# Kernel tuning notes

Hardware: AMD Instinct MI355X
Metric: run time of the kernel (lower is better)

## Reference

```python
import jax, jax.numpy as jnp
import numpy as np

# ---- constants mirroring init_kwargs ----
S = 128          # sheet_units
KA = 25          # aff_cf_units
C = 2            # aff_cf_channels
KL = 25          # lat_cf_units
EXC = 9          # exc_units
DA = 1           # aff_cf_dilation
DL = 1           # lat_cf_dilation
HOMEO_TARGET = 0.04
STRENGTH = 1.0

# ---- radial helper masks (get_circle / get_radial_cos) ----
def _dist(n):
    g = jnp.arange(n, dtype=jnp.float32) - (n - 1) / 2.0
    return jnp.sqrt(g[:, None] ** 2 + g[None, :] ** 2)

def _circle(n, r):
    return (_dist(n) < r).astype(jnp.float32)

def _rcos(n, wl):
    return jnp.cos(_dist(n) * jnp.pi / wl)

# afferent envelope: [C*KA*KA], channel-major like torch repeat+view
_ae = _rcos(KA, KA) ** 2 * _circle(KA, KA / 2)
_ae = _ae / _ae.max()
AFF_ENV = jnp.tile(_ae.reshape(1, KA * KA), (C, 1)).reshape(C * KA * KA)

# lateral (LRI) envelope: [KL*KL]
_inh = _rcos(KL, EXC / DL) ** 2 * _circle(KL, EXC / (2 * DL))
_le = _rcos(KL, KL) ** 2 * (1.0 - _inh) * _circle(KL, KL / 2)
LRI_ENV = (_le / _le.max()).reshape(KL * KL)

def _unfold(x, k, dil):
    """x: [C,H,W] -> patches [L, C*k*k], torch F.unfold ordering (C slowest)."""
    Cc, H, W = x.shape
    out = H - dil * (k - 1)
    idx = jnp.arange(out)[:, None] + dil * jnp.arange(k)[None, :]  # [out,k]
    p = x[:, idx, :]          # [C,out,k,W]
    p = p[:, :, :, idx]       # [C,out,k,out,k]
    p = p.transpose(1, 3, 0, 2, 4)  # [out_i,out_j,C,ki,kj]
    return p.reshape(out * out, Cc * k * k)

def setup_inputs() -> dict:
    key = jax.random.key(0)
    k1, k2 = jax.random.split(key)
    in_size = S + DA * (KA - 1)  # 152
    x = jax.random.uniform(k1, (1, C, in_size, in_size), dtype=jnp.float32)
    rfs = jax.random.uniform(k2, (S * S, C * KA * KA, 1), dtype=jnp.float32)
    rfs = rfs / rfs.sum(1, keepdims=True)
    lat_weights = jnp.ones((S * S, KL * KL, 1), jnp.float32) / (KL * KL)
    adathresh = jnp.zeros((1, 1, S, S), jnp.float32)
    return {"x": x, "rfs": rfs, "lat_weights": lat_weights, "adathresh": adathresh}

def _forward(x, rfs, lat_weights, adathresh):
    relu = jax.nn.relu
    rfs = relu(rfs)                 # no_grad positive clamp of params
    lw = relu(lat_weights)
    # afferent: unfold + envelope + per-pixel dot (bmm with [L,F,1])
    tiles = _unfold(x[0], KA, DA) * AFF_ENV[None, :]          # [L, C*KA*KA]
    raw_aff = jnp.einsum('lf,lf->l', tiles, rfs[:, :, 0]).reshape(S, S)
    aff = jax.lax.stop_gradient(raw_aff) - adathresh[0, 0]
    lat = relu(aff)
    # lateral inhibition: pad so unfold yields S*S positions
    p = DL * (KL - 1) // 2
    lt = _unfold(jnp.pad(lat, p)[None], KL, DL) * LRI_ENV[None, :]  # [L, KL*KL]
    lat_neg = jnp.einsum('lf,lf->l', lt, jax.lax.stop_gradient(lw)[:, :, 0]).reshape(S, S)
    lat = lat - lat_neg
    lat = jnp.tanh(relu(lat * STRENGTH + aff))
    # hebbian lateral correlations term (learning_flag path)
    lt2 = _unfold(jnp.pad(lat, p, constant_values=HOMEO_TARGET)[None], KL, DL) * LRI_ENV[None, :]
    weighted = lt2 * lat.reshape(S * S, 1)
    lat_correlations = jnp.einsum('lf,lf->', weighted, lw[:, :, 0])
    return (raw_aff.reshape(1, 1, S, S), lat.reshape(1, 1, S, S),
            lat_correlations, tiles[:, None, :])

def reference(x, rfs, lat_weights, adathresh):
    return _forward(x, rfs, lat_weights, adathresh)
```

## Files before the change

### kernel.cpp

```cpp
#include <hip/hip_runtime.h>
#include <math.h>

#define S 128
#define KA 25
#define KL 25
#define PATCH 625
#define FEAT 1250
#define PI_F 3.14159265358979323846f

#define WS_ENV 0
#define WS_LAT0 640
#define WS_PART 17024

__global__ __launch_bounds__(256) void k_tiles_aff(const float* __restrict__ x,
                                                   const float* __restrict__ rfs,
                                                   const float* __restrict__ ada,
                                                   float* __restrict__ raw_aff,
                                                   float* __restrict__ tiles,
                                                   float* __restrict__ ws) {
    __shared__ float s_ae[PATCH];
    __shared__ float s_part[8];
    const int tid = threadIdx.x;
    const int lane = tid & 63;
    const int wv = tid >> 6;

    for (int i = tid; i < PATCH; i += 256) {
        float di = (float)(i / KA) - 12.0f;
        float dj = (float)(i % KA) - 12.0f;
        float d = sqrtf(di * di + dj * dj);
        float v = 0.0f;
        if (d < 12.5f) { float c = cosf(d * (PI_F / 25.0f)); v = c * c; }
        s_ae[i] = v;
    }
    __syncthreads();

    const int p = blockIdx.x;
    const long pbase = (long)p * 2500;
    const float4* __restrict__ rfs4 = (const float4*)(rfs + pbase);
    float4* __restrict__ st4 = (float4*)(tiles + pbase - 1);

    float acc0 = 0.0f, acc1 = 0.0f;
    for (int k = tid; k < 625; k += 256) {
        float t[5];
#pragma unroll
        for (int e = 0; e < 5; ++e) {
            int fp = 4 * k - 1 + e;
            int u = fp + 1250;
            int li_ = u / 1250;
            int f = u - 1250 * li_;
            int l = 2 * p + li_ - 1;
            if (l < 0) l = 0;
            int c = f >= 625;
            int r = f - 625 * c;
            int ki = r / 25;
            int kj = r - 25 * ki;
            int li = l >> 7, lj = l & 127;
            t[e] = x[c * (152 * 152) + (li + ki) * 152 + (lj + kj)] * s_ae[r];
        }
        st4[k] = make_float4(t[0], t[1], t[2], t[3]);
        float4 rv = rfs4[k];
        if (4 * k + 3 < 1250) {
            acc0 += t[1] * fmaxf(rv.x, 0.f) + t[2] * fmaxf(rv.y, 0.f)
                  + t[3] * fmaxf(rv.z, 0.f) + t[4] * fmaxf(rv.w, 0.f);
        } else if (4 * k >= 1250) {
            acc1 += t[1] * fmaxf(rv.x, 0.f) + t[2] * fmaxf(rv.y, 0.f)
                  + t[3] * fmaxf(rv.z, 0.f) + t[4] * fmaxf(rv.w, 0.f);
        } else {
            acc0 += t[1] * fmaxf(rv.x, 0.f) + t[2] * fmaxf(rv.y, 0.f);
            acc1 += t[3] * fmaxf(rv.z, 0.f) + t[4] * fmaxf(rv.w, 0.f);
        }
    }

    if (p == 8191 && tid == 0) {
        tiles[pbase + 2499] = x[152 * 152 + 151 * 152 + 151] * s_ae[624];
    }

    for (int off = 32; off > 0; off >>= 1) {
        acc0 += __shfl_down(acc0, off);
        acc1 += __shfl_down(acc1, off);
    }
    if (lane == 0) { s_part[wv] = acc0; s_part[4 + wv] = acc1; }
    __syncthreads();
    if (tid == 0) {
        float ra0 = s_part[0] + s_part[1] + s_part[2] + s_part[3];
        float ra1 = s_part[4] + s_part[5] + s_part[6] + s_part[7];
        int l0 = 2 * p;
        raw_aff[l0] = ra0;
        raw_aff[l0 + 1] = ra1;
        ws[WS_LAT0 + l0] = fmaxf(ra0 - ada[l0], 0.0f);
        ws[WS_LAT0 + l0 + 1] = fmaxf(ra1 - ada[l0 + 1], 0.0f);
    }

    if (blockIdx.x == 0) {
        __syncthreads();
        float m = 0.0f;
        for (int i = tid; i < PATCH; i += 256) {
            float di = (float)(i / KL) - 12.0f;
            float dj = (float)(i % KL) - 12.0f;
            float d = sqrtf(di * di + dj * dj);
            float v = 0.0f;
            if (d < 12.5f) {
                float c1 = cosf(d * (PI_F / 25.0f));
                float inh = 0.0f;
                if (d < 4.5f) { float c2 = cosf(d * (PI_F / 9.0f)); inh = c2 * c2; }
                v = c1 * c1 * (1.0f - inh);
            }
            s_ae[i] = v;
            m = fmaxf(m, v);
        }
        for (int off = 32; off > 0; off >>= 1) m = fmaxf(m, __shfl_down(m, off));
        if (lane == 0) s_part[wv] = m;
        __syncthreads();
        float inv = 1.0f / fmaxf(fmaxf(s_part[0], s_part[1]),
                                 fmaxf(s_part[2], s_part[3]));
        for (int i = tid; i < PATCH; i += 256) ws[WS_ENV + i] = s_ae[i] * inv;
    }
}

__global__ __launch_bounds__(256) void k_lat(const float* __restrict__ raw_aff,
                                             const float* __restrict__ ada,
                                             const float* __restrict__ lw,
                                             float* __restrict__ latf,
                                             const float* __restrict__ ws) {
    __shared__ float s_le[PATCH];
    const int tid = threadIdx.x;
    for (int i = tid; i < PATCH; i += 256) s_le[i] = ws[WS_ENV + i];
    __syncthreads();

    const int lane = tid & 63;
    const int wv = tid >> 6;
    const int q = blockIdx.x * 4 + wv;
    const int l0 = q * 4;
    const float4* __restrict__ lw4 = (const float4*)(lw + (long)q * 2500);
    const float* __restrict__ lat0 = ws + WS_LAT0;

    float a0 = 0.f, a1 = 0.f, a2 = 0.f, a3 = 0.f;
    for (int k = lane; k < 625; k += 64) {
        float4 w4 = lw4[k];
        float w[4] = { w4.x, w4.y, w4.z, w4.w };
#pragma unroll
        for (int e = 0; e < 4; ++e) {
            int fp = 4 * k + e;
            int li_ = fp / 625;
            int r = fp - 625 * li_;
            int ki = r / 25;
            int kj = r - 25 * ki;
            int l = l0 + li_;
            int ri = (l >> 7) + ki - 12;
            int rj = (l & 127) + kj - 12;
            float lv = 0.0f;
            if (ri >= 0 && ri < S && rj >= 0 && rj < S) lv = lat0[ri * S + rj];
            float contrib = lv * s_le[r] * fmaxf(w[e], 0.0f);
            a0 += (li_ == 0) ? contrib : 0.0f;
            a1 += (li_ == 1) ? contrib : 0.0f;
            a2 += (li_ == 2) ? contrib : 0.0f;
            a3 += (li_ == 3) ? contrib : 0.0f;
        }
    }
    for (int off = 32; off > 0; off >>= 1) {
        a0 += __shfl_down(a0, off); a1 += __shfl_down(a1, off);
        a2 += __shfl_down(a2, off); a3 += __shfl_down(a3, off);
    }
    if (lane == 0) {
        float acc[4] = { a0, a1, a2, a3 };
#pragma unroll
        for (int j = 0; j < 4; ++j) {
            int l = l0 + j;
            float aff_l = raw_aff[l] - ada[l];
            float v = fmaxf(aff_l, 0.0f) - acc[j] + aff_l;
            latf[l] = tanhf(fmaxf(v, 0.0f));
        }
    }
}

__global__ __launch_bounds__(256) void k_corr(const float* __restrict__ latf,
                                              const float* __restrict__ lw,
                                              float* __restrict__ ws) {
    __shared__ float s_le[PATCH];
    __shared__ float s_part[4];
    const int tid = threadIdx.x;
    for (int i = tid; i < PATCH; i += 256) s_le[i] = ws[WS_ENV + i];
    __syncthreads();

    const int lane = tid & 63;
    const int wv = tid >> 6;
    const int q = blockIdx.x * 4 + wv;
    const int l0 = q * 4;
    const float4* __restrict__ lw4 = (const float4*)(lw + (long)q * 2500);

    float a0 = 0.f, a1 = 0.f, a2 = 0.f, a3 = 0.f;
    for (int k = lane; k < 625; k += 64) {
        float4 w4 = lw4[k];
        float w[4] = { w4.x, w4.y, w4.z, w4.w };
#pragma unroll
        for (int e = 0; e < 4; ++e) {
            int fp = 4 * k + e;
            int li_ = fp / 625;
            int r = fp - 625 * li_;
            int ki = r / 25;
            int kj = r - 25 * ki;
            int l = l0 + li_;
            int ri = (l >> 7) + ki - 12;
            int rj = (l & 127) + kj - 12;
            float lv = 0.04f;
            if (ri >= 0 && ri < S && rj >= 0 && rj < S) lv = latf[ri * S + rj];
            float contrib = lv * s_le[r] * fmaxf(w[e], 0.0f);
            a0 += (li_ == 0) ? contrib : 0.0f;
            a1 += (li_ == 1) ? contrib : 0.0f;
            a2 += (li_ == 2) ? contrib : 0.0f;
            a3 += (li_ == 3) ? contrib : 0.0f;
        }
    }
    for (int off = 32; off > 0; off >>= 1) {
        a0 += __shfl_down(a0, off); a1 += __shfl_down(a1, off);
        a2 += __shfl_down(a2, off); a3 += __shfl_down(a3, off);
    }
    if (lane == 0) {
        s_part[wv] = a0 * latf[l0] + a1 * latf[l0 + 1]
                   + a2 * latf[l0 + 2] + a3 * latf[l0 + 3];
    }
    __syncthreads();
    if (tid == 0)
        ws[WS_PART + blockIdx.x] = s_part[0] + s_part[1] + s_part[2] + s_part[3];
}

__global__ __launch_bounds__(256) void k_reduce(const float* __restrict__ ws,
                                                float* __restrict__ corr) {
    __shared__ float s_part[4];
    const int tid = threadIdx.x;
    const int lane = tid & 63;
    const int wv = tid >> 6;
    float acc = 0.0f;
    for (int i = tid; i < 1024; i += 256) acc += ws[WS_PART + i];
    for (int off = 32; off > 0; off >>= 1) acc += __shfl_down(acc, off);
    if (lane == 0) s_part[wv] = acc;
    __syncthreads();
    if (tid == 0) corr[0] = s_part[0] + s_part[1] + s_part[2] + s_part[3];
}

extern "C" void kernel_launch(void* const* d_in, const int* in_sizes, int n_in,
                              void* d_out, int out_size, void* d_ws, size_t ws_size,
                              hipStream_t stream) {
    const float* x   = (const float*)d_in[0];
    const float* rfs = (const float*)d_in[1];
    const float* lw  = (const float*)d_in[2];
    const float* ada = (const float*)d_in[3];

    float* out      = (float*)d_out;
    float* raw_aff  = out;
    float* latf     = out + S * S;
    float* corr     = out + 2 * S * S;
    float* tiles    = out + 2 * S * S + 1;
    float* ws       = (float*)d_ws;

    k_tiles_aff<<<(S * S) / 2, 256, 0, stream>>>(x, rfs, ada, raw_aff, tiles, ws);
    k_lat<<<(S * S) / 16, 256, 0, stream>>>(raw_aff, ada, lw, latf, ws);
    k_corr<<<(S * S) / 16, 256, 0, stream>>>(latf, lw, ws);
    k_reduce<<<1, 256, 0, stream>>>(ws, corr);
}
```

Measured before the change: 232.6 us.

## Precompute gather offsets/envelopes in setup kernel and use padded lateral grids

Result: slower. 251.2 us (+8.0%).

```diff
diff --git a/kernel.cpp b/kernel.cpp
--- a/kernel.cpp
+++ b/kernel.cpp
@@ -2,78 +2,118 @@
 #include <math.h>
 
 #define S 128
-#define KA 25
-#define KL 25
-#define PATCH 625
-#define FEAT 1250
 #define PI_F 3.14159265358979323846f
 
-#define WS_ENV 0
-#define WS_LAT0 640
-#define WS_PART 17024
+#define WS_T1OFF 0
+#define WS_T1AE  2500
+#define WS_T2OFF 5000
+#define WS_T2LE  7500
+#define WS_LAT0P 10000
+#define WS_LATP  33104
+#define WS_PART  56208
+
+__global__ __launch_bounds__(256) void k_setup(float* __restrict__ wsf) {
+    int* wsi = (int*)wsf;
+    const int tid = threadIdx.x;
+    __shared__ float s_le[625];
+    __shared__ float s_red[4];
+
+    float m = 0.0f;
+    for (int r = tid; r < 625; r += 256) {
+        float di = (float)(r / 25) - 12.0f;
+        float dj = (float)(r % 25) - 12.0f;
+        float d = sqrtf(di * di + dj * dj);
+        float v = 0.0f;
+        if (d < 12.5f) {
+            float c1 = cosf(d * (PI_F / 25.0f));
+            float inh = 0.0f;
+            if (d < 4.5f) { float c2 = cosf(d * (PI_F / 9.0f)); inh = c2 * c2; }
+            v = c1 * c1 * (1.0f - inh);
+        }
+        s_le[r] = v;
+        m = fmaxf(m, v);
+    }
+    for (int off = 32; off > 0; off >>= 1) m = fmaxf(m, __shfl_down(m, off));
+    if ((tid & 63) == 0) s_red[tid >> 6] = m;
+    __syncthreads();
+    const float inv = 1.0f / fmaxf(fmaxf(s_red[0], s_red[1]),
+                                   fmaxf(s_red[2], s_red[3]));
+
+    for (int fp = tid; fp < 2500; fp += 256) {
+        int half = fp >= 1250;
+        int f = fp - 1250 * half;
+        int c = f >= 625;
+        int r = f - 625 * c;
+        int ki = r / 25, kj = r - 25 * ki;
+        wsi[WS_T1OFF + fp] = c * 23104 + ki * 152 + kj + half;
+        float di = (float)ki - 12.0f, dj = (float)kj - 12.0f;
+        float d = sqrtf(di * di + dj * dj);
+        float ae = 0.0f;
+        if (d < 12.5f) { float cc = cosf(d * (PI_F / 25.0f)); ae = cc * cc; }
+        wsf[WS_T1AE + fp] = ae;
+        int li_ = fp / 625;
+        int r2 = fp - 625 * li_;
+        int ki2 = r2 / 25, kj2 = r2 - 25 * ki2;
+        wsi[WS_T2OFF + fp] = ki2 * 152 + kj2 + li_;
+        wsf[WS_T2LE + fp] = s_le[r2] * inv;
+    }
+    for (int i = tid; i < 23104; i += 256) {
+        wsf[WS_LAT0P + i] = 0.0f;
+        wsf[WS_LATP + i] = 0.04f;
+    }
+}
 
 __global__ __launch_bounds__(256) void k_tiles_aff(const float* __restrict__ x,
                                                    const float* __restrict__ rfs,
                                                    const float* __restrict__ ada,
                                                    float* __restrict__ raw_aff,
                                                    float* __restrict__ tiles,
-                                                   float* __restrict__ ws) {
-    __shared__ float s_ae[PATCH];
+                                                   float* __restrict__ wsf) {
+    __shared__ int   s_off[2500];
+    __shared__ float s_ae[2500];
     __shared__ float s_part[8];
+    const int* wsi = (const int*)wsf;
     const int tid = threadIdx.x;
     const int lane = tid & 63;
     const int wv = tid >> 6;
-
-    for (int i = tid; i < PATCH; i += 256) {
-        float di = (float)(i / KA) - 12.0f;
-        float dj = (float)(i % KA) - 12.0f;
-        float d = sqrtf(di * di + dj * dj);
-        float v = 0.0f;
-        if (d < 12.5f) { float c = cosf(d * (PI_F / 25.0f)); v = c * c; }
-        s_ae[i] = v;
+    for (int i = tid; i < 2500; i += 256) {
+        s_off[i] = wsi[WS_T1OFF + i];
+        s_ae[i] = wsf[WS_T1AE + i];
     }
     __syncthreads();
 
     const int p = blockIdx.x;
+    const int l0 = 2 * p;
+    const int li = l0 >> 7, lj = l0 & 127;
+    const float* __restrict__ xb = x + li * 152 + lj;
     const long pbase = (long)p * 2500;
     const float4* __restrict__ rfs4 = (const float4*)(rfs + pbase);
     float4* __restrict__ st4 = (float4*)(tiles + pbase - 1);
 
     float acc0 = 0.0f, acc1 = 0.0f;
     for (int k = tid; k < 625; k += 256) {
-        float t[5];
-#pragma unroll
-        for (int e = 0; e < 5; ++e) {
-            int fp = 4 * k - 1 + e;
-            int u = fp + 1250;
-            int li_ = u / 1250;
-            int f = u - 1250 * li_;
-            int l = 2 * p + li_ - 1;
-            if (l < 0) l = 0;
-            int c = f >= 625;
-            int r = f - 625 * c;
-            int ki = r / 25;
-            int kj = r - 25 * ki;
-            int li = l >> 7, lj = l & 127;
-            t[e] = x[c * (152 * 152) + (li + ki) * 152 + (lj + kj)] * s_ae[r];
+        int4 o4 = *(const int4*)(s_off + 4 * k);
+        float4 a4 = *(const float4*)(s_ae + 4 * k);
+        float t1 = xb[o4.x] * a4.x;
+        float t2 = xb[o4.y] * a4.y;
+        float t3 = xb[o4.z] * a4.z;
+        float t4 = xb[o4.w] * a4.w;
+        float t0 = __shfl_up(t4, 1);
+        if (lane == 0) {
+            t0 = 0.0f;
+            if (k > 0) t0 = xb[s_off[4 * k - 1]] * s_ae[4 * k - 1];
         }
-        st4[k] = make_float4(t[0], t[1], t[2], t[3]);
+        st4[k] = make_float4(t0, t1, t2, t3);
         float4 rv = rfs4[k];
-        if (4 * k + 3 < 1250) {
-            acc0 += t[1] * fmaxf(rv.x, 0.f) + t[2] * fmaxf(rv.y, 0.f)
-                  + t[3] * fmaxf(rv.z, 0.f) + t[4] * fmaxf(rv.w, 0.f);
-        } else if (4 * k >= 1250) {
-            acc1 += t[1] * fmaxf(rv.x, 0.f) + t[2] * fmaxf(rv.y, 0.f)
-                  + t[3] * fmaxf(rv.z, 0.f) + t[4] * fmaxf(rv.w, 0.f);
-        } else {
-            acc0 += t[1] * fmaxf(rv.x, 0.f) + t[2] * fmaxf(rv.y, 0.f);
-            acc1 += t[3] * fmaxf(rv.z, 0.f) + t[4] * fmaxf(rv.w, 0.f);
-        }
-    }
-
-    if (p == 8191 && tid == 0) {
-        tiles[pbase + 2499] = x[152 * 152 + 151 * 152 + 151] * s_ae[624];
-    }
+        float c0 = t1 * fmaxf(rv.x, 0.f), c1 = t2 * fmaxf(rv.y, 0.f);
+        float c2 = t3 * fmaxf(rv.z, 0.f), c3 = t4 * fmaxf(rv.w, 0.f);
+        int fp = 4 * k;
+        acc0 += (fp < 1250 ? c0 : 0.f) + (fp + 1 < 1250 ? c1 : 0.f)
+              + (fp + 2 < 1250 ? c2 : 0.f) + (fp + 3 < 1250 ? c3 : 0.f);
+        acc1 += (fp >= 1250 ? c0 : 0.f) + (fp + 1 >= 1250 ? c1 : 0.f)
+              + (fp + 2 >= 1250 ? c2 : 0.f) + (fp + 3 >= 1250 ? c3 : 0.f);
+    }
+    if (p == 8191 && tid == 0) tiles[pbase + 2499] = 0.0f;
 
     for (int off = 32; off > 0; off >>= 1) {
         acc0 += __shfl_down(acc0, off);
@@ -84,78 +124,54 @@
     if (tid == 0) {
         float ra0 = s_part[0] + s_part[1] + s_part[2] + s_part[3];
         float ra1 = s_part[4] + s_part[5] + s_part[6] + s_part[7];
-        int l0 = 2 * p;
         raw_aff[l0] = ra0;
         raw_aff[l0 + 1] = ra1;
-        ws[WS_LAT0 + l0] = fmaxf(ra0 - ada[l0], 0.0f);
-        ws[WS_LAT0 + l0 + 1] = fmaxf(ra1 - ada[l0 + 1], 0.0f);
-    }
-
-    if (blockIdx.x == 0) {
-        __syncthreads();
-        float m = 0.0f;
-        for (int i = tid; i < PATCH; i += 256) {
-            float di = (float)(i / KL) - 12.0f;
-            float dj = (float)(i % KL) - 12.0f;
-            float d = sqrtf(di * di + dj * dj);
-            float v = 0.0f;
-            if (d < 12.5f) {
-                float c1 = cosf(d * (PI_F / 25.0f));
-                float inh = 0.0f;
-                if (d < 4.5f) { float c2 = cosf(d * (PI_F / 9.0f)); inh = c2 * c2; }
-                v = c1 * c1 * (1.0f - inh);
-            }
-            s_ae[i] = v;
-            m = fmaxf(m, v);
-        }
-        for (int off = 32; off > 0; off >>= 1) m = fmaxf(m, __shfl_down(m, off));
-        if (lane == 0) s_part[wv] = m;
-        __syncthreads();
-        float inv = 1.0f / fmaxf(fmaxf(s_part[0], s_part[1]),
-                                 fmaxf(s_part[2], s_part[3]));
-        for (int i = tid; i < PATCH; i += 256) ws[WS_ENV + i] = s_ae[i] * inv;
-    }
-}
+        wsf[WS_LAT0P + (li + 12) * 152 + (lj + 12)] = fmaxf(ra0 - ada[l0], 0.0f);
+        wsf[WS_LAT0P + (li + 12) * 152 + (lj + 13)] = fmaxf(ra1 - ada[l0 + 1], 0.0f);
+    }
+}
+
+#define SEL4(fp_, c_)                                                     \
+    {                                                                     \
+        a0 += ((fp_) < 625) ? (c_) : 0.0f;                                \
+        a1 += ((fp_) >= 625 && (fp_) < 1250) ? (c_) : 0.0f;               \
+        a2 += ((fp_) >= 1250 && (fp_) < 1875) ? (c_) : 0.0f;              \
+        a3 += ((fp_) >= 1875) ? (c_) : 0.0f;                              \
+    }
 
 __global__ __launch_bounds__(256) void k_lat(const float* __restrict__ raw_aff,
                                              const float* __restrict__ ada,
                                              const float* __restrict__ lw,
                                              float* __restrict__ latf,
-                                             const float* __restrict__ ws) {
-    __shared__ float s_le[PATCH];
-    const int tid = threadIdx.x;
-    for (int i = tid; i < PATCH; i += 256) s_le[i] = ws[WS_ENV + i];
-    __syncthreads();
-
-    const int lane = tid & 63;
-    const int wv = tid >> 6;
+                                             float* __restrict__ wsf) {
+    __shared__ int   s_off[2500];
+    __shared__ float s_le[2500];
+    const int* wsi = (const int*)wsf;
+    const int tid = threadIdx.x;
+    for (int i = tid; i < 2500; i += 256) {
+        s_off[i] = wsi[WS_T2OFF + i];
+        s_le[i] = wsf[WS_T2LE + i];
+    }
+    __syncthreads();
+
+    const int lane = tid & 63, wv = tid >> 6;
     const int q = blockIdx.x * 4 + wv;
-    const int l0 = q * 4;
+    const int l0 = 4 * q;
+    const int li = l0 >> 7, lj = l0 & 127;
+    const float* __restrict__ g = wsf + WS_LAT0P + li * 152 + lj;
     const float4* __restrict__ lw4 = (const float4*)(lw + (long)q * 2500);
-    const float* __restrict__ lat0 = ws + WS_LAT0;
 
     float a0 = 0.f, a1 = 0.f, a2 = 0.f, a3 = 0.f;
     for (int k = lane; k < 625; k += 64) {
+        int4 o4 = *(const int4*)(s_off + 4 * k);
+        float4 e4 = *(const float4*)(s_le + 4 * k);
         float4 w4 = lw4[k];
-        float w[4] = { w4.x, w4.y, w4.z, w4.w };
-#pragma unroll
-        for (int e = 0; e < 4; ++e) {
-            int fp = 4 * k + e;
-            int li_ = fp / 625;
-            int r = fp - 625 * li_;
-            int ki = r / 25;
-            int kj = r - 25 * ki;
-            int l = l0 + li_;
-            int ri = (l >> 7) + ki - 12;
-            int rj = (l & 127) + kj - 12;
-            float lv = 0.0f;
-            if (ri >= 0 && ri < S && rj >= 0 && rj < S) lv = lat0[ri * S + rj];
-            float contrib = lv * s_le[r] * fmaxf(w[e], 0.0f);
-            a0 += (li_ == 0) ? contrib : 0.0f;
-            a1 += (li_ == 1) ? contrib : 0.0f;
-            a2 += (li_ == 2) ? contrib : 0.0f;
-            a3 += (li_ == 3) ? contrib : 0.0f;
-        }
+        float c0 = g[o4.x] * e4.x * fmaxf(w4.x, 0.f);
+        float c1 = g[o4.y] * e4.y * fmaxf(w4.y, 0.f);
+        float c2 = g[o4.z] * e4.z * fmaxf(w4.z, 0.f);
+        float c3 = g[o4.w] * e4.w * fmaxf(w4.w, 0.f);
+        int fp = 4 * k;
+        SEL4(fp, c0); SEL4(fp + 1, c1); SEL4(fp + 2, c2); SEL4(fp + 3, c3);
     }
     for (int off = 32; off > 0; off >>= 1) {
         a0 += __shfl_down(a0, off); a1 += __shfl_down(a1, off);
@@ -168,48 +184,45 @@
             int l = l0 + j;
             float aff_l = raw_aff[l] - ada[l];
             float v = fmaxf(aff_l, 0.0f) - acc[j] + aff_l;
-            latf[l] = tanhf(fmaxf(v, 0.0f));
+            float lf = tanhf(fmaxf(v, 0.0f));
+            latf[l] = lf;
+            wsf[WS_LATP + (li + 12) * 152 + (lj + 12 + j)] = lf;
         }
     }
 }
 
 __global__ __launch_bounds__(256) void k_corr(const float* __restrict__ latf,
                                               const float* __restrict__ lw,
-                                              float* __restrict__ ws) {
-    __shared__ float s_le[PATCH];
+                                              float* __restrict__ wsf) {
+    __shared__ int   s_off[2500];
+    __shared__ float s_le[2500];
     __shared__ float s_part[4];
-    const int tid = threadIdx.x;
-    for (int i = tid; i < PATCH; i += 256) s_le[i] = ws[WS_ENV + i];
-    __syncthreads();
-
-    const int lane = tid & 63;
-    const int wv = tid >> 6;
+    const int* wsi = (const int*)wsf;
+    const int tid = threadIdx.x;
+    for (int i = tid; i < 2500; i += 256) {
+        s_off[i] = wsi[WS_T2OFF + i];
+        s_le[i] = wsf[WS_T2LE + i];
+    }
+    __syncthreads();
+
+    const int lane = tid & 63, wv = tid >> 6;
     const int q = blockIdx.x * 4 + wv;
-    const int l0 = q * 4;
+    const int l0 = 4 * q;
+    const int li = l0 >> 7, lj = l0 & 127;
+    const float* __restrict__ g = wsf + WS_LATP + li * 152 + lj;
     const float4* __restrict__ lw4 = (const float4*)(lw + (long)q * 2500);
 
     float a0 = 0.f, a1 = 0.f, a2 = 0.f, a3 = 0.f;
     for (int k = lane; k < 625; k += 64) {
+        int4 o4 = *(const int4*)(s_off + 4 * k);
+        float4 e4 = *(const float4*)(s_le + 4 * k);
         float4 w4 = lw4[k];
-        float w[4] = { w4.x, w4.y, w4.z, w4.w };
-#pragma unroll
-        for (int e = 0; e < 4; ++e) {
-            int fp = 4 * k + e;
-            int li_ = fp / 625;
-            int r = fp - 625 * li_;
-            int ki = r / 25;
-            int kj = r - 25 * ki;
-            int l = l0 + li_;
-            int ri = (l >> 7) + ki - 12;
-            int rj = (l & 127) + kj - 12;
-            float lv = 0.04f;
-            if (ri >= 0 && ri < S && rj >= 0 && rj < S) lv = latf[ri * S + rj];
-            float contrib = lv * s_le[r] * fmaxf(w[e], 0.0f);
-            a0 += (li_ == 0) ? contrib : 0.0f;
-            a1 += (li_ == 1) ? contrib : 0.0f;
-            a2 += (li_ == 2) ? contrib : 0.0f;
-            a3 += (li_ == 3) ? contrib : 0.0f;
-        }
+        float c0 = g[o4.x] * e4.x * fmaxf(w4.x, 0.f);
+        float c1 = g[o4.y] * e4.y * fmaxf(w4.y, 0.f);
+        float c2 = g[o4.z] * e4.z * fmaxf(w4.z, 0.f);
+        float c3 = g[o4.w] * e4.w * fmaxf(w4.w, 0.f);
+        int fp = 4 * k;
+        SEL4(fp, c0); SEL4(fp + 1, c1); SEL4(fp + 2, c2); SEL4(fp + 3, c3);
     }
     for (int off = 32; off > 0; off >>= 1) {
         a0 += __shfl_down(a0, off); a1 += __shfl_down(a1, off);
@@ -221,17 +234,16 @@
     }
     __syncthreads();
     if (tid == 0)
-        ws[WS_PART + blockIdx.x] = s_part[0] + s_part[1] + s_part[2] + s_part[3];
-}
-
-__global__ __launch_bounds__(256) void k_reduce(const float* __restrict__ ws,
+        wsf[WS_PART + blockIdx.x] = s_part[0] + s_part[1] + s_part[2] + s_part[3];
+}
+
+__global__ __launch_bounds__(256) void k_reduce(const float* __restrict__ wsf,
                                                 float* __restrict__ corr) {
     __shared__ float s_part[4];
     const int tid = threadIdx.x;
-    const int lane = tid & 63;
-    const int wv = tid >> 6;
+    const int lane = tid & 63, wv = tid >> 6;
     float acc = 0.0f;
-    for (int i = tid; i < 1024; i += 256) acc += ws[WS_PART + i];
+    for (int i = tid; i < 1024; i += 256) acc += wsf[WS_PART + i];
     for (int off = 32; off > 0; off >>= 1) acc += __shfl_down(acc, off);
     if (lane == 0) s_part[wv] = acc;
     __syncthreads();
@@ -246,13 +258,14 @@
     const float* lw  = (const float*)d_in[2];
     const float* ada = (const float*)d_in[3];
 
-    float* out      = (float*)d_out;
-    float* raw_aff  = out;
-    float* latf     = out + S * S;
-    float* corr     = out + 2 * S * S;
-    float* tiles    = out + 2 * S * S + 1;
-    float* ws       = (float*)d_ws;
-
+    float* out     = (float*)d_out;
+    float* raw_aff = out;
+    float* latf    = out + S * S;
+    float* corr    = out + 2 * S * S;
+    float* tiles   = out + 2 * S * S + 1;
+    float* ws      = (float*)d_ws;
+
+    k_setup<<<1, 256, 0, stream>>>(ws);
     k_tiles_aff<<<(S * S) / 2, 256, 0, stream>>>(x, rfs, ada, raw_aff, tiles, ws);
     k_lat<<<(S * S) / 16, 256, 0, stream>>>(raw_aff, ada, lw, latf, ws);
     k_corr<<<(S * S) / 16, 256, 0, stream>>>(latf, lw, ws);
```
